# Optimization experiments

Hardware: AMD Instinct MI355X
Metric: run time of the kernel (lower is better)

## Reference

```python
import jax, jax.numpy as jnp
import numpy as np

D_MODEL = 1024
N_HEADS = 16
D_HEAD = D_MODEL // N_HEADS
WINDOW = 256
ATTN_SCALE = 1.0
SCALE = float(np.sqrt(D_HEAD))
NEG = -10000.0


def setup_inputs() -> dict:
    key = jax.random.key(0)
    ks = jax.random.split(key, 7)
    B, S = 2, 2048
    q = jax.random.normal(ks[0], (B, S, D_MODEL), dtype=jnp.float32)
    k = jax.random.normal(ks[1], (B, S, D_MODEL), dtype=jnp.float32)
    v = jax.random.normal(ks[2], (B, S, D_MODEL), dtype=jnp.float32)
    # Xavier-uniform-like scale for square linear weights: sqrt(6/(fan_in+fan_out))
    lim = float(np.sqrt(6.0 / (D_MODEL + D_MODEL)))
    def xavier(kk):
        return jax.random.uniform(kk, (D_MODEL, D_MODEL), minval=-lim, maxval=lim, dtype=jnp.float32)
    return {"q": q, "k": k, "v": v,
            "WQ": xavier(ks[3]), "WK": xavier(ks[4]),
            "WV": xavier(ks[5]), "WO": xavier(ks[6])}


def _split_heads(x):
    B, S, _ = x.shape
    return x.reshape(B, S, N_HEADS, D_HEAD).transpose(0, 2, 1, 3)  # [B,H,S,Dh]


def reference(q, k, v, WQ, WK, WV, WO):
    B, Sq, _ = q.shape
    Sk = k.shape[1]
    # torch nn.Linear: y = x @ W.T
    qh = _split_heads(q @ WQ.T) / SCALE          # [B,H,Sq,Dh]
    kh = _split_heads(k @ WK.T)                  # [B,H,Sk,Dh]
    vh = _split_heads(v @ WV.T)                  # [B,H,Sk,Dh]
    scores = jnp.einsum('bhqd,bhkd->bhqk', qh, kh) * ATTN_SCALE
    # global abs-max normalization (clamped at 1)
    scores = scores / jnp.maximum(jnp.max(jnp.abs(scores)), 1.0)
    # sliding window mask: key j visible to query i iff i-WINDOW+1 <= j <= i
    qi = jnp.arange(Sq)[:, None]
    kj = jnp.arange(Sk)[None, :]
    win = (kj <= qi) & (kj > qi - WINDOW)        # [Sq,Sk] bool
    scores = jnp.where(win[None, None], scores, NEG)
    attn = jax.nn.softmax(scores, axis=-1)
    out = jnp.einsum('bhqk,bhkd->bhqd', attn, vh)
    out = out.transpose(0, 2, 1, 3).reshape(B, Sq, D_MODEL)
    out = out @ WO.T
    out = out / jnp.maximum(jnp.mean(jnp.abs(out)), 1.0)
    return out
```

## Files before the change

kernel.cpp:

```cpp
#include <hip/hip_runtime.h>
#include <hip/hip_bf16.h>

#define S_LEN 2048
#define DM    1024
#define NH    16
#define DH    64
#define WIN   256
#define BATCH 2

using f32x4   = __attribute__((ext_vector_type(4))) float;
using bf16x8  = __attribute__((ext_vector_type(8))) short;
using ushort8 = __attribute__((ext_vector_type(8))) unsigned short;

static __device__ __forceinline__ unsigned short f2bf(float f) {
  unsigned int x = __float_as_uint(f);
  x += 0x7fffu + ((x >> 16) & 1u);
  return (unsigned short)(x >> 16);
}

typedef const __attribute__((address_space(1))) void* gas_t;
typedef __attribute__((address_space(3))) void* las_t;
static __device__ __forceinline__ void gload16(const void* g, void* l) {
  __builtin_amdgcn_global_load_lds((gas_t)g, (las_t)l, 16, 0, 0);
}

__global__ __launch_bounds__(256) void k_cvt_all(const float* __restrict__ w0,
                                                 const float* __restrict__ w1,
                                                 const float* __restrict__ w2,
                                                 const float* __restrict__ w3,
                                                 const float* __restrict__ q,
                                                 const float* __restrict__ k,
                                                 const float* __restrict__ v,
                                                 unsigned short* __restrict__ Wb,
                                                 unsigned short* __restrict__ qb,
                                                 unsigned short* __restrict__ kb,
                                                 unsigned short* __restrict__ vb,
                                                 unsigned int* __restrict__ absmax) {
  const int z = blockIdx.z;
  if (z == 0 && blockIdx.x == 0 && threadIdx.x == 0) *absmax = 0u;
  const float* src;
  unsigned short* dst;
  int n8;
  if (z < 4) {
    src = (z == 0) ? w0 : (z == 1) ? w1 : (z == 2) ? w2 : w3;
    dst = Wb + (size_t)z * DM * DM;
    n8 = (DM * DM) / 8;
  } else {
    src = (z == 4) ? q : (z == 5) ? k : v;
    dst = (z == 4) ? qb : (z == 5) ? kb : vb;
    n8 = (BATCH * S_LEN * DM) / 8;
  }
  int i = blockIdx.x * blockDim.x + threadIdx.x;
  int stride = gridDim.x * blockDim.x;
  for (; i < n8; i += stride) {
    float4 f0 = ((const float4*)src)[2 * i];
    float4 f1 = ((const float4*)src)[2 * i + 1];
    ushort8 u;
    u[0] = f2bf(f0.x); u[1] = f2bf(f0.y); u[2] = f2bf(f0.z); u[3] = f2bf(f0.w);
    u[4] = f2bf(f1.x); u[5] = f2bf(f1.y); u[6] = f2bf(f1.z); u[7] = f2bf(f1.w);
    ((ushort8*)dst)[i] = u;
  }
}

__device__ __forceinline__ void gemm128_core(const unsigned short* __restrict__ A,
                                             const unsigned short* __restrict__ Bw,
                                             void* __restrict__ Cptr, float oscale,
                                             int omode, bool swap, int R0, int C0,
                                             float* __restrict__ partials, int pbid) {
  __shared__ unsigned short As[2][128][64];
  __shared__ unsigned short Bs[2][128][64];
  __shared__ float red[4];
  const int tid = threadIdx.x, lane = tid & 63, w = tid >> 6;
  const int wr = w >> 1, wc = w & 1;

  int srow[4], scol[4];
#pragma unroll
  for (int c = 0; c < 4; ++c) {
    srow[c] = c * 32 + w * 8 + (lane >> 3);
    scol[c] = ((lane & 7) ^ (srow[c] & 7)) << 3;
  }

  f32x4 z = {0.f, 0.f, 0.f, 0.f};
  f32x4 acc[4][4];
#pragma unroll
  for (int i = 0; i < 4; ++i)
#pragma unroll
    for (int j = 0; j < 4; ++j) acc[i][j] = z;

  unsigned short* Af0 = &As[0][0][0];
  unsigned short* Bf0 = &Bs[0][0][0];
  const int cb = 16 * (lane >> 4);

#define STAGE_G(buf, k0) do {                                                          \
    unsigned short* Ad = Af0 + (buf) * 8192 + w * 512;                                 \
    unsigned short* Bd = Bf0 + (buf) * 8192 + w * 512;                                 \
    _Pragma("unroll")                                                                  \
    for (int c = 0; c < 4; ++c) {                                                      \
      gload16(A  + (size_t)(R0 + srow[c]) * DM + (k0) + scol[c], Ad + c * 2048);       \
      gload16(Bw + (size_t)(C0 + srow[c]) * DM + (k0) + scol[c], Bd + c * 2048);       \
    }                                                                                  \
  } while (0)

  STAGE_G(0, 0);
  __syncthreads();

  for (int t = 0; t < 16; ++t) {
    const int cur = t & 1;
    if (t + 1 < 16) STAGE_G(cur ^ 1, (t + 1) * 64);

    const char* Af = (const char*)(Af0 + cur * 8192);
    const char* Bf = (const char*)(Bf0 + cur * 8192);
    bf16x8 av[4][2], bv[4][2];
#pragma unroll
    for (int i = 0; i < 4; ++i) {
      int row = 64 * wr + 16 * i + (lane & 15);
      int sw = (row & 7) << 4;
      const char* rp = Af + row * 128;
      av[i][0] = *(const bf16x8*)(rp + (cb ^ sw));
      av[i][1] = *(const bf16x8*)(rp + ((cb + 64) ^ sw));
    }
#pragma unroll
    for (int j = 0; j < 4; ++j) {
      int row = 64 * wc + 16 * j + (lane & 15);
      int sw = (row & 7) << 4;
      const char* rp = Bf + row * 128;
      bv[j][0] = *(const bf16x8*)(rp + (cb ^ sw));
      bv[j][1] = *(const bf16x8*)(rp + ((cb + 64) ^ sw));
    }
    if (swap) {
#pragma unroll
      for (int i = 0; i < 4; ++i)
#pragma unroll
        for (int j = 0; j < 4; ++j) {
          acc[i][j] = __builtin_amdgcn_mfma_f32_16x16x32_bf16(bv[j][0], av[i][0], acc[i][j], 0, 0, 0);
          acc[i][j] = __builtin_amdgcn_mfma_f32_16x16x32_bf16(bv[j][1], av[i][1], acc[i][j], 0, 0, 0);
        }
    } else {
#pragma unroll
      for (int i = 0; i < 4; ++i)
#pragma unroll
        for (int j = 0; j < 4; ++j) {
          acc[i][j] = __builtin_amdgcn_mfma_f32_16x16x32_bf16(av[i][0], bv[j][0], acc[i][j], 0, 0, 0);
          acc[i][j] = __builtin_amdgcn_mfma_f32_16x16x32_bf16(av[i][1], bv[j][1], acc[i][j], 0, 0, 0);
        }
    }
    __syncthreads();
  }
#undef STAGE_G

  float s = 0.f;
#pragma unroll
  for (int i = 0; i < 4; ++i) {
#pragma unroll
    for (int j = 0; j < 4; ++j) {
      if (swap) {
        int grow  = R0 + 64 * wr + 16 * i + (lane & 15);
        int gcol0 = C0 + 64 * wc + 16 * j + 4 * (lane >> 4);
        if (omode == 0) {
          float4 st = {acc[i][j][0] * oscale, acc[i][j][1] * oscale,
                       acc[i][j][2] * oscale, acc[i][j][3] * oscale};
          s += fabsf(st.x) + fabsf(st.y) + fabsf(st.z) + fabsf(st.w);
          *(float4*)((float*)Cptr + (size_t)grow * DM + gcol0) = st;
        } else {
          int b = grow >> 11, ss = grow & (S_LEN - 1);
          int h = gcol0 >> 6, d0 = gcol0 & 63;
          ushort4 st = {f2bf(acc[i][j][0] * oscale), f2bf(acc[i][j][1] * oscale),
                        f2bf(acc[i][j][2] * oscale), f2bf(acc[i][j][3] * oscale)};
          *(ushort4*)((unsigned short*)Cptr + (((size_t)(b * NH + h) * S_LEN + ss) << 6) + d0) = st;
        }
      } else {
        int grow0 = R0 + 64 * wr + 16 * i + 4 * (lane >> 4);
        int gcol  = C0 + 64 * wc + 16 * j + (lane & 15);
        int b = grow0 >> 11, s0 = grow0 & (S_LEN - 1);
        int h = gcol >> 6, d = gcol & 63;
        ushort4 st = {f2bf(acc[i][j][0] * oscale), f2bf(acc[i][j][1] * oscale),
                      f2bf(acc[i][j][2] * oscale), f2bf(acc[i][j][3] * oscale)};
        *(ushort4*)((unsigned short*)Cptr + (((size_t)(b * NH + h) * DH + d) << 11) + s0) = st;
      }
    }
  }
  if (partials) {
#pragma unroll
    for (int mk = 1; mk < 64; mk <<= 1) s += __shfl_xor(s, mk, 64);
    if (lane == 0) red[w] = s;
    __syncthreads();
    if (tid == 0) partials[pbid] = red[0] + red[1] + red[2] + red[3];
  }
}

__global__ __launch_bounds__(256) void k_gemm_qkv(const unsigned short* __restrict__ qb,
                                                  const unsigned short* __restrict__ kb,
                                                  const unsigned short* __restrict__ vb,
                                                  const unsigned short* __restrict__ WbQ,
                                                  const unsigned short* __restrict__ WbK,
                                                  const unsigned short* __restrict__ WbV,
                                                  unsigned short* __restrict__ qh,
                                                  unsigned short* __restrict__ kh,
                                                  unsigned short* __restrict__ vt) {
  const unsigned short *A, *B;
  unsigned short* C;
  float sc;
  int om;
  bool sw;
  if (blockIdx.z == 0)      { A = qb; B = WbQ; C = qh; sc = 0.125f; om = 1; sw = true;  }
  else if (blockIdx.z == 1) { A = kb; B = WbK; C = kh; sc = 1.0f;   om = 1; sw = true;  }
  else                      { A = vb; B = WbV; C = vt; sc = 1.0f;   om = 2; sw = false; }
  gemm128_core(A, B, C, sc, om, sw, blockIdx.x * 128, blockIdx.y * 128, nullptr, 0);
}

__global__ __launch_bounds__(256) void k_gemm_out(const unsigned short* __restrict__ A,
                                                  const unsigned short* __restrict__ Bw,
                                                  float* __restrict__ C,
                                                  float* __restrict__ partials) {
  gemm128_core(A, Bw, C, 1.0f, 0, true, blockIdx.x * 128, blockIdx.y * 128,
               partials, blockIdx.x + gridDim.x * blockIdx.y);
}

__global__ __launch_bounds__(256) void k_scoresmax(const unsigned short* __restrict__ qh,
                                                   const unsigned short* __restrict__ kh,
                                                   unsigned int* __restrict__ absmax) {
  __shared__ unsigned short Ks[2][128][64];
  const int tid = threadIdx.x, lane = tid & 63, w = tid >> 6;
  const size_t base = (size_t)blockIdx.y * S_LEN * DH;
  const unsigned short* Q = qh + base;
  const unsigned short* K = kh + base;
  const int q0 = blockIdx.x * 128;

  bf16x8 a[2][2];
#pragma unroll
  for (int rb = 0; rb < 2; ++rb) {
    const unsigned short* qr = Q + (size_t)(q0 + 32 * w + 16 * rb + (lane & 15)) * DH + 8 * (lane >> 4);
    a[rb][0] = *(const bf16x8*)qr;
    a[rb][1] = *(const bf16x8*)(qr + 32);
  }

  int srow[4], scol[4];
#pragma unroll
  for (int c = 0; c < 4; ++c) {
    srow[c] = c * 32 + w * 8 + (lane >> 3);
    scol[c] = ((lane & 7) ^ (srow[c] & 7)) << 3;
  }
  unsigned short* Kf0 = &Ks[0][0][0];
  const int cbb = 16 * (lane >> 4);

#define STAGE_K(buf, kc) do {                                                          \
    unsigned short* Kd = Kf0 + (buf) * 8192 + w * 512;                                 \
    _Pragma("unroll")                                                                  \
    for (int c = 0; c < 4; ++c)                                                        \
      gload16(K + (size_t)((kc) + srow[c]) * DH + scol[c], Kd + c * 2048);             \
  } while (0)

  STAGE_K(0, 0);
  __syncthreads();

  float m = 0.f;
  for (int t = 0; t < 16; ++t) {
    const int cur = t & 1;
    if (t + 1 < 16) STAGE_K(cur ^ 1, (t + 1) * 128);
    const char* Kf = (const char*)(Kf0 + cur * 8192);
#pragma unroll
    for (int cb = 0; cb < 8; ++cb) {
      int row = 16 * cb + (lane & 15);
      int sw = (row & 7) << 4;
      const char* rp = Kf + row * 128;
      bf16x8 b0 = *(const bf16x8*)(rp + (cbb ^ sw));
      bf16x8 b1 = *(const bf16x8*)(rp + ((cbb + 64) ^ sw));
#pragma unroll
      for (int rb = 0; rb < 2; ++rb) {
        f32x4 acc = {0.f, 0.f, 0.f, 0.f};
        acc = __builtin_amdgcn_mfma_f32_16x16x32_bf16(a[rb][0], b0, acc, 0, 0, 0);
        acc = __builtin_amdgcn_mfma_f32_16x16x32_bf16(a[rb][1], b1, acc, 0, 0, 0);
        m = fmaxf(m, fmaxf(fmaxf(fabsf(acc[0]), fabsf(acc[1])), fmaxf(fabsf(acc[2]), fabsf(acc[3]))));
      }
    }
    __syncthreads();
  }
#undef STAGE_K

#pragma unroll
  for (int mk = 1; mk < 64; mk <<= 1) m = fmaxf(m, __shfl_xor(m, mk, 64));
  __shared__ float red[4];
  if (lane == 0) red[w] = m;
  __syncthreads();
  if (threadIdx.x == 0)
    atomicMax(absmax, __float_as_uint(fmaxf(fmaxf(red[0], red[1]), fmaxf(red[2], red[3]))));
}

#define NT 10
__global__ __launch_bounds__(256) void k_attn(const unsigned short* __restrict__ qh,
                                              const unsigned short* __restrict__ kh,
                                              const unsigned short* __restrict__ vt,
                                              const unsigned int* __restrict__ absmax,
                                              unsigned short* __restrict__ attn_c) {
  __shared__ unsigned short Ks[2][32][72];
  __shared__ unsigned short Vts[2][64][40];
  __shared__ unsigned short Pl[4][16][40];
  const int tid = threadIdx.x, lane = tid & 63, w = tid >> 6;
  const int bh = blockIdx.y, b = bh >> 4, h = bh & 15;
  const int Q0 = blockIdx.x * 64;
  const int kstart = Q0 - WIN;
  const size_t base = (size_t)bh * S_LEN * DH;
  const unsigned short* Kb = kh + base;
  const unsigned short* Vtb = vt + base;

  const int skrow = tid >> 3, skcol = (tid & 7) << 3;
  const int svd = tid >> 2, svcol = (tid & 3) << 3;

  const float invM = 1.0f / fmaxf(__uint_as_float(*absmax), 1.0f);
  const unsigned short* Qp = qh + base + (size_t)(Q0 + 16 * w + (lane & 15)) * DH + 8 * (lane >> 4);
  bf16x8 a0 = *(const bf16x8*)Qp;
  bf16x8 a1 = *(const bf16x8*)(Qp + 32);

  ushort8 rk, rv;
  ushort8 zz = {0, 0, 0, 0, 0, 0, 0, 0};
#define LOADT(T) do {                                                        \
    int kk = kstart + 32 * (T) + skrow;                                      \
    rk = (kk >= 0) ? *(const ushort8*)(Kb + (size_t)kk * DH + skcol) : zz;   \
    int kc = kstart + 32 * (T) + svcol;                                      \
    rv = (kc >= 0) ? *(const ushort8*)(Vtb + (size_t)svd * S_LEN + kc) : zz; \
  } while (0)
#define WRITET(buf) do {                                                     \
    *(ushort8*)&Ks[buf][skrow][skcol] = rk;                                  \
    *(ushort8*)&Vts[buf][svd][svcol] = rv;                                   \
  } while (0)

  LOADT(0);
  WRITET(0);
  __syncthreads();

  const int Tlo = w >> 1, Thi = (w >> 1) + 8;
  const int qrow = Q0 + 16 * w + 4 * (lane >> 4);
  float sm[4] = {0.f, 0.f, 0.f, 0.f};
  f32x4 z = {0.f, 0.f, 0.f, 0.f};
  f32x4 o[4];
#pragma unroll
  for (int i = 0; i < 4; ++i) o[i] = z;

  for (int T = 0; T < NT; ++T) {
    const int cur = T & 1;
    const bool act = (T >= Tlo) && (T <= Thi);
    if (T + 1 < NT) LOADT(T + 1);
    if (act) {
      f32x4 p[2];
#pragma unroll
      for (int cb = 0; cb < 2; ++cb) {
        const unsigned short* kr = &Ks[cur][16 * cb + (lane & 15)][8 * (lane >> 4)];
        bf16x8 b0 = *(const bf16x8*)kr;
        bf16x8 b1 = *(const bf16x8*)(kr + 32);
        f32x4 a = z;
        a = __builtin_amdgcn_mfma_f32_16x16x32_bf16(a0, b0, a, 0, 0, 0);
        a = __builtin_amdgcn_mfma_f32_16x16x32_bf16(a1, b1, a, 0, 0, 0);
        p[cb] = a;
      }
#pragma unroll
      for (int cb = 0; cb < 2; ++cb) {
        int kcol = kstart + 32 * T + 16 * cb + (lane & 15);
#pragma unroll
        for (int r = 0; r < 4; ++r) {
          int qq = qrow + r;
          bool ok = (kcol >= 0) && (kcol <= qq) && (kcol + WIN > qq);
          float e = ok ? __expf(p[cb][r] * invM) : 0.f;
          sm[r] += e;
          Pl[w][4 * (lane >> 4) + r][16 * cb + (lane & 15)] = f2bf(e);
        }
      }
    }
    __syncthreads();
    if (act) {
      bf16x8 pa = *(const bf16x8*)&Pl[w][lane & 15][8 * (lane >> 4)];
#pragma unroll
      for (int dt = 0; dt < 4; ++dt) {
        bf16x8 bv = *(const bf16x8*)&Vts[cur][16 * dt + (lane & 15)][8 * (lane >> 4)];
        o[dt] = __builtin_amdgcn_mfma_f32_16x16x32_bf16(pa, bv, o[dt], 0, 0, 0);
      }
    }
    if (T + 1 < NT) WRITET((T + 1) & 1);
    __syncthreads();
  }

#pragma unroll
  for (int r = 0; r < 4; ++r) {
#pragma unroll
    for (int mk = 1; mk < 16; mk <<= 1) sm[r] += __shfl_xor(sm[r], mk, 64);
    sm[r] = 1.0f / sm[r];
  }
#pragma unroll
  for (int dt = 0; dt < 4; ++dt) {
#pragma unroll
    for (int r = 0; r < 4; ++r) {
      int qq = qrow + r;
      float val = o[dt][r] * sm[r];
      attn_c[((size_t)(b * S_LEN + qq) << 10) + h * DH + 16 * dt + (lane & 15)] = f2bf(val);
    }
  }
#undef LOADT
#undef WRITET
}

__global__ __launch_bounds__(256) void k_scale_final(float* __restrict__ x,
                                                     const float* __restrict__ partials,
                                                     float invcnt, int n4) {
  __shared__ float red[4];
  float s = partials[threadIdx.x];
#pragma unroll
  for (int mk = 1; mk < 64; mk <<= 1) s += __shfl_xor(s, mk, 64);
  if ((threadIdx.x & 63) == 0) red[threadIdx.x >> 6] = s;
  __syncthreads();
  float d = 1.0f / fmaxf((red[0] + red[1] + red[2] + red[3]) * invcnt, 1.0f);
  for (int i = blockIdx.x * blockDim.x + threadIdx.x; i < n4; i += gridDim.x * blockDim.x) {
    float4 f = ((float4*)x)[i];
    f.x *= d; f.y *= d; f.z *= d; f.w *= d;
    ((float4*)x)[i] = f;
  }
}

extern "C" void kernel_launch(void* const* d_in, const int* in_sizes, int n_in,
                              void* d_out, int out_size, void* d_ws, size_t ws_size,
                              hipStream_t stream) {
  (void)in_sizes; (void)n_in; (void)out_size; (void)ws_size;
  const float* q  = (const float*)d_in[0];
  const float* k  = (const float*)d_in[1];
  const float* v  = (const float*)d_in[2];
  const float* WQ = (const float*)d_in[3];
  const float* WK = (const float*)d_in[4];
  const float* WV = (const float*)d_in[5];
  const float* WO = (const float*)d_in[6];

  const size_t HS = (size_t)BATCH * NH * S_LEN * DH;
  unsigned short* qb     = (unsigned short*)d_ws;
  unsigned short* kb     = qb + HS;
  unsigned short* vb     = kb + HS;
  unsigned short* qh     = vb + HS;
  unsigned short* kh     = qh + HS;
  unsigned short* vt     = kh + HS;
  unsigned short* Wb     = vt + HS;
  char* scal             = (char*)(Wb + 4 * (size_t)DM * DM);
  unsigned int* absmax   = (unsigned int*)scal;
  float* partials        = (float*)(scal + 16);
  unsigned short* attn_c = qb;

  unsigned short* WbQ = Wb;
  unsigned short* WbK = Wb + (size_t)DM * DM;
  unsigned short* WbV = Wb + 2 * (size_t)DM * DM;
  unsigned short* WbO = Wb + 3 * (size_t)DM * DM;

  k_cvt_all<<<dim3(128, 1, 7), 256, 0, stream>>>(WQ, WK, WV, WO, q, k, v, Wb, qb, kb, vb, absmax);

  k_gemm_qkv<<<dim3(32, 8, 3), 256, 0, stream>>>(qb, kb, vb, WbQ, WbK, WbV, qh, kh, vt);

  k_scoresmax<<<dim3(16, 32), 256, 0, stream>>>(qh, kh, absmax);
  k_attn<<<dim3(32, 32), 256, 0, stream>>>(qh, kh, vt, absmax, attn_c);

  k_gemm_out<<<dim3(32, 8), 256, 0, stream>>>(attn_c, WbO, (float*)d_out, partials);

  k_scale_final<<<1024, 256, 0, stream>>>((float*)d_out, partials, 1.0f / (float)HS, (int)(HS / 4));
}
```

Baseline: 138.0 us.

## Fuse output mean-abs scaling into out-projection GEMM via grid barrier

Removes the separate scale pass over the output. The out-projection GEMM now publishes per-block abs-sums, waits at a global atomic-counter barrier, then applies the normalization before its single store. This avoids one full read-modify-write of the 16 MB output and one kernel launch. It relies on all 256 blocks being co-resident, or the spin barrier deadlocks. The scores-max kernel also now handles 256 query rows per block instead of 128, halving its grid.

```diff
diff --git a/kernel.cpp b/kernel.cpp
--- a/kernel.cpp
+++ b/kernel.cpp
@@ -35,9 +35,10 @@
                                                  unsigned short* __restrict__ qb,
                                                  unsigned short* __restrict__ kb,
                                                  unsigned short* __restrict__ vb,
-                                                 unsigned int* __restrict__ absmax) {
+                                                 unsigned int* __restrict__ absmax,
+                                                 unsigned int* __restrict__ counter) {
   const int z = blockIdx.z;
-  if (z == 0 && blockIdx.x == 0 && threadIdx.x == 0) *absmax = 0u;
+  if (z == 0 && blockIdx.x == 0 && threadIdx.x == 0) { *absmax = 0u; *counter = 0u; }
   const float* src;
   unsigned short* dst;
   int n8;
@@ -66,7 +67,9 @@
                                              const unsigned short* __restrict__ Bw,
                                              void* __restrict__ Cptr, float oscale,
                                              int omode, bool swap, int R0, int C0,
-                                             float* __restrict__ partials, int pbid) {
+                                             float* __restrict__ partials,
+                                             unsigned int* __restrict__ counter,
+                                             int pbid, int nblocks, float invcnt) {
   __shared__ unsigned short As[2][128][64];
   __shared__ unsigned short Bs[2][128][64];
   __shared__ float red[4];
@@ -148,7 +151,48 @@
   }
 #undef STAGE_G
 
-  float s = 0.f;
+  if (omode == 0) {
+    float s = 0.f;
+#pragma unroll
+    for (int i = 0; i < 4; ++i)
+#pragma unroll
+      for (int j = 0; j < 4; ++j)
+#pragma unroll
+        for (int r = 0; r < 4; ++r) s += fabsf(acc[i][j][r] * oscale);
+#pragma unroll
+    for (int mk = 1; mk < 64; mk <<= 1) s += __shfl_xor(s, mk, 64);
+    if (lane == 0) red[w] = s;
+    __syncthreads();
+    if (tid == 0) {
+      float bs = red[0] + red[1] + red[2] + red[3];
+      __hip_atomic_store(&partials[pbid], bs, __ATOMIC_RELAXED, __HIP_MEMORY_SCOPE_AGENT);
+      __threadfence();
+      atomicAdd(counter, 1u);
+      while (__hip_atomic_load(counter, __ATOMIC_RELAXED, __HIP_MEMORY_SCOPE_AGENT) < (unsigned)nblocks)
+        __builtin_amdgcn_s_sleep(2);
+    }
+    __syncthreads();
+    __threadfence();
+    float ps = __hip_atomic_load(&partials[tid], __ATOMIC_RELAXED, __HIP_MEMORY_SCOPE_AGENT);
+#pragma unroll
+    for (int mk = 1; mk < 64; mk <<= 1) ps += __shfl_xor(ps, mk, 64);
+    if (lane == 0) red[w] = ps;
+    __syncthreads();
+    const float d = 1.0f / fmaxf((red[0] + red[1] + red[2] + red[3]) * invcnt, 1.0f);
+#pragma unroll
+    for (int i = 0; i < 4; ++i) {
+#pragma unroll
+      for (int j = 0; j < 4; ++j) {
+        int grow  = R0 + 64 * wr + 16 * i + (lane & 15);
+        int gcol0 = C0 + 64 * wc + 16 * j + 4 * (lane >> 4);
+        float4 st = {acc[i][j][0] * oscale * d, acc[i][j][1] * oscale * d,
+                     acc[i][j][2] * oscale * d, acc[i][j][3] * oscale * d};
+        *(float4*)((float*)Cptr + (size_t)grow * DM + gcol0) = st;
+      }
+    }
+    return;
+  }
+
 #pragma unroll
   for (int i = 0; i < 4; ++i) {
 #pragma unroll
@@ -156,18 +200,11 @@
       if (swap) {
         int grow  = R0 + 64 * wr + 16 * i + (lane & 15);
         int gcol0 = C0 + 64 * wc + 16 * j + 4 * (lane >> 4);
-        if (omode == 0) {
-          float4 st = {acc[i][j][0] * oscale, acc[i][j][1] * oscale,
-                       acc[i][j][2] * oscale, acc[i][j][3] * oscale};
-          s += fabsf(st.x) + fabsf(st.y) + fabsf(st.z) + fabsf(st.w);
-          *(float4*)((float*)Cptr + (size_t)grow * DM + gcol0) = st;
-        } else {
-          int b = grow >> 11, ss = grow & (S_LEN - 1);
-          int h = gcol0 >> 6, d0 = gcol0 & 63;
-          ushort4 st = {f2bf(acc[i][j][0] * oscale), f2bf(acc[i][j][1] * oscale),
-                        f2bf(acc[i][j][2] * oscale), f2bf(acc[i][j][3] * oscale)};
-          *(ushort4*)((unsigned short*)Cptr + (((size_t)(b * NH + h) * S_LEN + ss) << 6) + d0) = st;
-        }
+        int b = grow >> 11, ss = grow & (S_LEN - 1);
+        int h = gcol0 >> 6, d0 = gcol0 & 63;
+        ushort4 st = {f2bf(acc[i][j][0] * oscale), f2bf(acc[i][j][1] * oscale),
+                      f2bf(acc[i][j][2] * oscale), f2bf(acc[i][j][3] * oscale)};
+        *(ushort4*)((unsigned short*)Cptr + (((size_t)(b * NH + h) * S_LEN + ss) << 6) + d0) = st;
       } else {
         int grow0 = R0 + 64 * wr + 16 * i + 4 * (lane >> 4);
         int gcol  = C0 + 64 * wc + 16 * j + (lane & 15);
@@ -178,13 +215,6 @@
         *(ushort4*)((unsigned short*)Cptr + (((size_t)(b * NH + h) * DH + d) << 11) + s0) = st;
       }
     }
-  }
-  if (partials) {
-#pragma unroll
-    for (int mk = 1; mk < 64; mk <<= 1) s += __shfl_xor(s, mk, 64);
-    if (lane == 0) red[w] = s;
-    __syncthreads();
-    if (tid == 0) partials[pbid] = red[0] + red[1] + red[2] + red[3];
   }
 }
 
@@ -205,15 +235,19 @@
   if (blockIdx.z == 0)      { A = qb; B = WbQ; C = qh; sc = 0.125f; om = 1; sw = true;  }
   else if (blockIdx.z == 1) { A = kb; B = WbK; C = kh; sc = 1.0f;   om = 1; sw = true;  }
   else                      { A = vb; B = WbV; C = vt; sc = 1.0f;   om = 2; sw = false; }
-  gemm128_core(A, B, C, sc, om, sw, blockIdx.x * 128, blockIdx.y * 128, nullptr, 0);
+  gemm128_core(A, B, C, sc, om, sw, blockIdx.x * 128, blockIdx.y * 128,
+               nullptr, nullptr, 0, 0, 0.f);
 }
 
 __global__ __launch_bounds__(256) void k_gemm_out(const unsigned short* __restrict__ A,
                                                   const unsigned short* __restrict__ Bw,
                                                   float* __restrict__ C,
-                                                  float* __restrict__ partials) {
+                                                  float* __restrict__ partials,
+                                                  unsigned int* __restrict__ counter,
+                                                  float invcnt) {
   gemm128_core(A, Bw, C, 1.0f, 0, true, blockIdx.x * 128, blockIdx.y * 128,
-               partials, blockIdx.x + gridDim.x * blockIdx.y);
+               partials, counter, blockIdx.x + gridDim.x * blockIdx.y,
+               gridDim.x * gridDim.y, invcnt);
 }
 
 __global__ __launch_bounds__(256) void k_scoresmax(const unsigned short* __restrict__ qh,
@@ -224,12 +258,12 @@
   const size_t base = (size_t)blockIdx.y * S_LEN * DH;
   const unsigned short* Q = qh + base;
   const unsigned short* K = kh + base;
-  const int q0 = blockIdx.x * 128;
-
-  bf16x8 a[2][2];
-#pragma unroll
-  for (int rb = 0; rb < 2; ++rb) {
-    const unsigned short* qr = Q + (size_t)(q0 + 32 * w + 16 * rb + (lane & 15)) * DH + 8 * (lane >> 4);
+  const int q0 = blockIdx.x * 256;
+
+  bf16x8 a[4][2];
+#pragma unroll
+  for (int rb = 0; rb < 4; ++rb) {
+    const unsigned short* qr = Q + (size_t)(q0 + 64 * w + 16 * rb + (lane & 15)) * DH + 8 * (lane >> 4);
     a[rb][0] = *(const bf16x8*)qr;
     a[rb][1] = *(const bf16x8*)(qr + 32);
   }
@@ -266,7 +300,7 @@
       bf16x8 b0 = *(const bf16x8*)(rp + (cbb ^ sw));
       bf16x8 b1 = *(const bf16x8*)(rp + ((cbb + 64) ^ sw));
 #pragma unroll
-      for (int rb = 0; rb < 2; ++rb) {
+      for (int rb = 0; rb < 4; ++rb) {
         f32x4 acc = {0.f, 0.f, 0.f, 0.f};
         acc = __builtin_amdgcn_mfma_f32_16x16x32_bf16(a[rb][0], b0, acc, 0, 0, 0);
         acc = __builtin_amdgcn_mfma_f32_16x16x32_bf16(a[rb][1], b1, acc, 0, 0, 0);
@@ -397,23 +431,6 @@
 #undef WRITET
 }
 
-__global__ __launch_bounds__(256) void k_scale_final(float* __restrict__ x,
-                                                     const float* __restrict__ partials,
-                                                     float invcnt, int n4) {
-  __shared__ float red[4];
-  float s = partials[threadIdx.x];
-#pragma unroll
-  for (int mk = 1; mk < 64; mk <<= 1) s += __shfl_xor(s, mk, 64);
-  if ((threadIdx.x & 63) == 0) red[threadIdx.x >> 6] = s;
-  __syncthreads();
-  float d = 1.0f / fmaxf((red[0] + red[1] + red[2] + red[3]) * invcnt, 1.0f);
-  for (int i = blockIdx.x * blockDim.x + threadIdx.x; i < n4; i += gridDim.x * blockDim.x) {
-    float4 f = ((float4*)x)[i];
-    f.x *= d; f.y *= d; f.z *= d; f.w *= d;
-    ((float4*)x)[i] = f;
-  }
-}
-
 extern "C" void kernel_launch(void* const* d_in, const int* in_sizes, int n_in,
                               void* d_out, int out_size, void* d_ws, size_t ws_size,
                               hipStream_t stream) {
@@ -436,6 +453,7 @@
   unsigned short* Wb     = vt + HS;
   char* scal             = (char*)(Wb + 4 * (size_t)DM * DM);
   unsigned int* absmax   = (unsigned int*)scal;
+  unsigned int* counter  = (unsigned int*)(scal + 8);
   float* partials        = (float*)(scal + 16);
   unsigned short* attn_c = qb;
 
@@ -444,14 +462,14 @@
   unsigned short* WbV = Wb + 2 * (size_t)DM * DM;
   unsigned short* WbO = Wb + 3 * (size_t)DM * DM;
 
-  k_cvt_all<<<dim3(128, 1, 7), 256, 0, stream>>>(WQ, WK, WV, WO, q, k, v, Wb, qb, kb, vb, absmax);
+  k_cvt_all<<<dim3(128, 1, 7), 256, 0, stream>>>(WQ, WK, WV, WO, q, k, v, Wb, qb, kb, vb,
+                                                 absmax, counter);
 
   k_gemm_qkv<<<dim3(32, 8, 3), 256, 0, stream>>>(qb, kb, vb, WbQ, WbK, WbV, qh, kh, vt);
 
-  k_scoresmax<<<dim3(16, 32), 256, 0, stream>>>(qh, kh, absmax);
+  k_scoresmax<<<dim3(8, 32), 256, 0, stream>>>(qh, kh, absmax);
   k_attn<<<dim3(32, 32), 256, 0, stream>>>(qh, kh, vt, absmax, attn_c);
 
-  k_gemm_out<<<dim3(32, 8), 256, 0, stream>>>(attn_c, WbO, (float*)d_out, partials);
-
-  k_scale_final<<<1024, 256, 0, stream>>>((float*)d_out, partials, 1.0f / (float)HS, (int)(HS / 4));
-}
+  k_gemm_out<<<dim3(32, 8), 256, 0, stream>>>(attn_c, WbO, (float*)d_out, partials, counter,
+                                              1.0f / (float)HS);
+}
```

Result: slower. 161.8 us (+17.2%).
